# Optimization experiments

Measured on AMD Instinct MI355X. Metric: run time of the kernel, lower is better.

## Reference

```python
import jax, jax.numpy as jnp
import numpy as np

B, N, C = 8, 8192, 256
H, D, S = 8, 32, 32          # heads, dim_head, slice_num
HID = 4 * C                  # mlp hidden


def layernorm(x, w, b, eps=1e-5):
    mu = jnp.mean(x, axis=-1, keepdims=True)
    var = jnp.mean(jnp.square(x - mu), axis=-1, keepdims=True)
    return (x - mu) * jax.lax.rsqrt(var + eps) * w + b


def setup_inputs() -> dict:
    key = jax.random.key(0)
    ks = jax.random.split(key, 16)
    s = lambda fan: 1.0 / np.sqrt(fan)
    return {
        "fx": jax.random.normal(ks[0], (B, N, C), jnp.float32),
        "ln1_w": jnp.ones((C,), jnp.float32),
        "ln1_b": jnp.zeros((C,), jnp.float32),
        "Wx": jax.random.uniform(ks[1], (C, C), jnp.float32, -s(C), s(C)),   # in_project_x weight [inner,dim]
        "bx": jax.random.uniform(ks[2], (C,), jnp.float32, -s(C), s(C)),
        "Wq": jax.random.uniform(ks[3], (S, D), jnp.float32, -s(D), s(D)),
        "Wk": jax.random.uniform(ks[4], (S, D), jnp.float32, -s(D), s(D)),
        "Wv": jax.random.uniform(ks[5], (D, D), jnp.float32, -s(D), s(D)),
        "Wo": jax.random.uniform(ks[6], (C, C), jnp.float32, -s(C), s(C)),   # to_out weight [dim,inner]
        "bo": jax.random.uniform(ks[7], (C,), jnp.float32, -s(C), s(C)),
        "ln2_w": jnp.ones((C,), jnp.float32),
        "ln2_b": jnp.zeros((C,), jnp.float32),
        "W1": jax.random.uniform(ks[8], (HID, C), jnp.float32, -s(C), s(C)),
        "b1": jax.random.uniform(ks[9], (HID,), jnp.float32, -s(C), s(C)),
        "W2": jax.random.uniform(ks[10], (C, HID), jnp.float32, -s(HID), s(HID)),
        "b2": jax.random.uniform(ks[11], (C,), jnp.float32, -s(HID), s(HID)),
    }


def linear_no_attn(x, Wx, bx, Wq, Wk, Wv, Wo, bo):
    # x: [B,N,C]
    x_mid = x @ Wx.T + bx                                   # [B,N,C]
    x_mid = x_mid.reshape(x.shape[0], x.shape[1], H, D).transpose(0, 2, 1, 3)  # [B,H,N,D]
    q = jax.nn.softmax(x_mid @ Wq.T, axis=-1)               # [B,H,N,S], softmax over slices
    k = jax.nn.softmax(x_mid @ Wk.T, axis=-2)               # [B,H,N,S], softmax over tokens
    v = x_mid @ Wv.T                                        # [B,H,N,D]
    kv = jnp.einsum('bhns,bhnd->bhsd', k, v)                # [B,H,S,D]
    qkv = jnp.einsum('bhns,bhsd->bhnd', q, kv)              # [B,H,N,D]
    qkv = qkv.transpose(0, 2, 1, 3).reshape(x.shape[0], x.shape[1], H * D)
    return qkv @ Wo.T + bo


def reference(fx, ln1_w, ln1_b, Wx, bx, Wq, Wk, Wv, Wo, bo, ln2_w, ln2_b, W1, b1, W2, b2):
    h = linear_no_attn(layernorm(fx, ln1_w, ln1_b), Wx, bx, Wq, Wk, Wv, Wo, bo) + fx
    y = layernorm(h, ln2_w, ln2_b)
    y = jax.nn.gelu(y @ W1.T + b1, approximate=False)       # MLP: pre + exact GELU, n_layers=0
    y = y @ W2.T + b2
    return y + h
```

## Files before the change

kernel.cpp:

```cpp
#include <hip/hip_runtime.h>
#include <math.h>


typedef __attribute__((ext_vector_type(8))) short bf8;
typedef __attribute__((ext_vector_type(4))) float f32x4;
typedef __attribute__((ext_vector_type(4))) unsigned short u16x4;
typedef __attribute__((ext_vector_type(8))) unsigned short u16x8;

__device__ __forceinline__ float b2f(unsigned short x) {
  union { unsigned u; float f; } t; t.u = ((unsigned)x) << 16; return t.f;
}
__device__ __forceinline__ unsigned short f2b(float f) {
  union { float f; unsigned u; } t; t.f = f;
  unsigned r = t.u + 0x7fffu + ((t.u >> 16) & 1u);
  return (unsigned short)(r >> 16);
}
__device__ __forceinline__ float gelu_exact(float x) {
  return 0.5f * x * (1.0f + erff(x * 0.7071067811865475f));
}
__device__ __forceinline__ float erf_fast(float x) {
  float ax = fabsf(x);
  float t = __builtin_amdgcn_rcpf(fmaf(0.3275911f, ax, 1.0f));
  float p = t * fmaf(t, fmaf(t, fmaf(t, fmaf(t, 1.061405429f, -1.453152027f),
                                     1.421413741f), -0.284496736f), 0.254829592f);
  float r = 1.0f - p * __expf(-ax * ax);
  return copysignf(r, x);
}
__device__ __forceinline__ float gelu_fast(float x) {
  return 0.5f * x * (1.0f + erf_fast(x * 0.7071067811865475f));
}

typedef __attribute__((address_space(1))) const void gas_void;
typedef __attribute__((address_space(3))) void las_void;
__device__ __forceinline__ void gl_lds16(const void* g, void* l) {
  __builtin_amdgcn_global_load_lds((gas_void*)g, (las_void*)l, 16, 0, 0);
}

__global__ void sniff_kernel(const unsigned* __restrict__ fx, int* __restrict__ flag,
                             unsigned* __restrict__ gate) {
  if (threadIdx.x == 0) {
    int cnt = 0;
    for (int i = 0; i < 64; i++) {
      unsigned e = (fx[i] >> 7) & 0xFFu;
      cnt += (e >= 117u && e <= 130u) ? 1 : 0;
    }
    *flag = (cnt >= 32) ? 1 : 0;
    *gate = 0u;
  }
}

struct CvtDesc { const void* src[15]; int off[15]; int n[15]; };

__global__ __launch_bounds__(256) void cvt_tab(CvtDesc d, unsigned short* __restrict__ wtab,
                                               const int* __restrict__ flagp) {
  const int seg = blockIdx.y;
  const int i = blockIdx.x * 256 + threadIdx.x;
  if (i >= d.n[seg]) return;
  unsigned short o;
  if (*flagp) o = ((const unsigned short*)d.src[seg])[i];
  else        o = f2b(((const float*)d.src[seg])[i]);
  wtab[d.off[seg] + i] = o;
}

__global__ __launch_bounds__(256) void build_big(
    const unsigned short* __restrict__ wq, const unsigned short* __restrict__ wk,
    unsigned short* __restrict__ Wqbig, unsigned short* __restrict__ Wkbig)
{
  const int idx = blockIdx.x * 256 + threadIdx.x;
  const int row = idx >> 8, col = idx & 255;
  const bool same = (row >> 5) == (col >> 5);
  const int wi = (row & 31) * 32 + (col & 31);
  Wqbig[idx] = same ? wq[wi] : (unsigned short)0;
  Wkbig[idx] = same ? wk[wi] : (unsigned short)0;
}

__global__ __launch_bounds__(256) void zero_u16(unsigned short* __restrict__ p, int n) {
  int i8 = (blockIdx.x * 256 + threadIdx.x) * 8;
  if (i8 < n) { u16x8 z = {}; *(u16x8*)&p[i8] = z; }
}

__global__ __launch_bounds__(256) void ln_stats(
    const void* __restrict__ X, const int* __restrict__ flagp, int amode,
    float* __restrict__ MU, float* __restrict__ RS)
{
  const int lane = threadIdx.x & 63;
  const int wave = threadIdx.x >> 6;
  const size_t row = (size_t)blockIdx.x * 4 + wave;
  const size_t base = row * 256 + lane * 4;
  const bool abf = amode ? ((*flagp) != 0) : true;
  float x0, x1, x2, x3;
  if (abf) {
    u16x4 uv = *(const u16x4*)&((const unsigned short*)X)[base];
    x0 = b2f(uv[0]); x1 = b2f(uv[1]); x2 = b2f(uv[2]); x3 = b2f(uv[3]);
  } else {
    f32x4 t = *(const f32x4*)&((const float*)X)[base];
    x0 = t[0]; x1 = t[1]; x2 = t[2]; x3 = t[3];
  }
  float s = x0 + x1 + x2 + x3;
  float q = x0*x0 + x1*x1 + x2*x2 + x3*x3;
  #pragma unroll
  for (int m = 1; m < 64; m <<= 1) { s += __shfl_xor(s, m, 64); q += __shfl_xor(q, m, 64); }
  float mean = s * (1.0f / 256.0f);
  float var  = q * (1.0f / 256.0f) - mean * mean;
  if (lane == 0) { MU[row] = mean; RS[row] = rsqrtf(var + 1e-5f); }
}

__global__ __launch_bounds__(256) void gemm_bt(
    const unsigned short* __restrict__ A,
    const unsigned short* __restrict__ W,
    const unsigned short* __restrict__ bias,
    const void* __restrict__ Res, const int* __restrict__ flagp,
    unsigned short* __restrict__ Y,
    int N, int K, int act, int mz, long wz)
{
  __shared__ __align__(16) unsigned short smem[3 * 8192];
  const int tid = threadIdx.x, lane = tid & 63, wave = tid >> 6;
  const size_t zrow = (size_t)blockIdx.z * mz;
  const int bm = blockIdx.x * 128, bn = blockIdx.y * 128;
  const int wm = (wave >> 1) * 64, wn = (wave & 1) * 64;
  const int quad = lane >> 4, l16 = lane & 15;
  const unsigned short* Wz = W + (size_t)blockIdx.z * wz;

  f32x4 acc[4][4] = {};
  const int r0 = tid >> 2;
  const int co = (tid & 3) * 8;
  const unsigned short* pa0 = &A[(zrow + bm + r0) * K + co];
  const unsigned short* pa1 = &A[(zrow + bm + r0 + 64) * K + co];
  const unsigned short* pb0 = &Wz[(size_t)(bn + r0) * K + co];
  const unsigned short* pb1 = &Wz[(size_t)(bn + r0 + 64) * K + co];
  const int nt = K >> 5;

  auto stage = [&](int t, int sl) {
    const int k0 = t << 5;
    unsigned short* b_ = &smem[sl * 8192 + tid * 8];
    gl_lds16(pa0 + k0, b_);
    gl_lds16(pa1 + k0, b_ + 2048);
    gl_lds16(pb0 + k0, b_ + 4096);
    gl_lds16(pb1 + k0, b_ + 6144);
  };

  stage(0, 0);
  if (nt > 1) stage(1, 1);
  int scur = 0, snew = 2;
  for (int t = 0; t < nt; ++t) {
    if (t + 2 < nt) {
      stage(t + 2, snew);
      asm volatile("s_waitcnt vmcnt(8)" ::: "memory");
    } else if (t + 1 < nt) {
      asm volatile("s_waitcnt vmcnt(4)" ::: "memory");
    } else {
      asm volatile("s_waitcnt vmcnt(0)" ::: "memory");
    }
    __builtin_amdgcn_s_barrier();
    __builtin_amdgcn_sched_barrier(0);

    const unsigned short* sa = &smem[scur * 8192];
    const unsigned short* sb = sa + 4096;
    bf8 af[4], bfr[4];
    #pragma unroll
    for (int i = 0; i < 4; i++) af[i]  = *(const bf8*)&sa[(wm + i * 16 + l16) * 32 + quad * 8];
    #pragma unroll
    for (int j = 0; j < 4; j++) bfr[j] = *(const bf8*)&sb[(wn + j * 16 + l16) * 32 + quad * 8];
    #pragma unroll
    for (int i = 0; i < 4; i++)
      #pragma unroll
      for (int j = 0; j < 4; j++)
        acc[i][j] = __builtin_amdgcn_mfma_f32_16x16x32_bf16(af[i], bfr[j], acc[i][j], 0, 0, 0);

    __builtin_amdgcn_sched_barrier(0);
    __builtin_amdgcn_s_barrier();
    scur = scur + 1 < 3 ? scur + 1 : 0;
    snew = snew + 1 < 3 ? snew + 1 : 0;
  }

  const bool rbf = Res ? ((*flagp) != 0) : true;
  float bv[4];
  #pragma unroll
  for (int j = 0; j < 4; j++) bv[j] = b2f(bias[bn + wn + j * 16 + l16]);
  #pragma unroll
  for (int i = 0; i < 4; i++)
    #pragma unroll
    for (int j = 0; j < 4; j++)
      #pragma unroll
      for (int r = 0; r < 4; r++) {
        float v = acc[i][j][r] + bv[j];
        if (act == 2) v = __expf(v);
        acc[i][j][r] = v;
      }
  if (act == 3) {
    #pragma unroll
    for (int i = 0; i < 4; i++)
      #pragma unroll
      for (int g = 0; g < 2; g++)
        #pragma unroll
        for (int r = 0; r < 4; r++) {
          float a0 = acc[i][2*g][r], a1 = acc[i][2*g+1][r];
          float m = fmaxf(a0, a1);
          #pragma unroll
          for (int msk = 1; msk < 16; msk <<= 1) m = fmaxf(m, __shfl_xor(m, msk, 64));
          float e0 = __expf(a0 - m), e1 = __expf(a1 - m);
          float s = e0 + e1;
          #pragma unroll
          for (int msk = 1; msk < 16; msk <<= 1) s += __shfl_xor(s, msk, 64);
          const float rz = 1.0f / s;
          acc[i][2*g][r] = e0 * rz; acc[i][2*g+1][r] = e1 * rz;
        }
  }

  float* cf = (float*)smem;
  const int whalf = wm >> 6;
  #pragma unroll
  for (int half = 0; half < 2; ++half) {
    __builtin_amdgcn_s_barrier();
    if (whalf == half) {
      #pragma unroll
      for (int i = 0; i < 4; i++)
        #pragma unroll
        for (int j = 0; j < 4; j++)
          #pragma unroll
          for (int r = 0; r < 4; r++)
            cf[(i * 16 + quad * 4 + r) * 132 + wn + j * 16 + l16] = acc[i][j][r];
    }
    __builtin_amdgcn_s_barrier();
    #pragma unroll
    for (int st = 0; st < 4; ++st) {
      const int e = st * 2048 + tid * 8;
      const int row = e >> 7;
      const int col = e & 127;
      const size_t gbase = (zrow + bm + half * 64 + row) * (size_t)N + bn + col;
      float v[8];
      #pragma unroll
      for (int u = 0; u < 8; u++) v[u] = cf[row * 132 + col + u];
      if (Res) {
        if (rbf) {
          u16x8 rv = *(const u16x8*)&((const unsigned short*)Res)[gbase];
          #pragma unroll
          for (int u = 0; u < 8; u++) v[u] += b2f(rv[u]);
        } else {
          f32x4 ra = *(const f32x4*)&((const float*)Res)[gbase];
          f32x4 rb = *(const f32x4*)&((const float*)Res)[gbase + 4];
          v[0] += ra[0]; v[1] += ra[1]; v[2] += ra[2]; v[3] += ra[3];
          v[4] += rb[0]; v[5] += rb[1]; v[6] += rb[2]; v[7] += rb[3];
        }
      }
      u16x8 o;
      #pragma unroll
      for (int u = 0; u < 8; u++) o[u] = f2b(v[u]);
      *(u16x8*)&Y[gbase] = o;
    }
  }
}

__global__ __launch_bounds__(256) void gemm_bt_ln(
    const void* __restrict__ A, const int* __restrict__ flagp, int amode,
    const float* __restrict__ MU, const float* __restrict__ RS,
    const unsigned short* __restrict__ lw, const unsigned short* __restrict__ lb,
    const unsigned short* __restrict__ W, const unsigned short* __restrict__ bias,
    unsigned short* __restrict__ Y, int N, int K, int act)
{
  __shared__ __align__(16) unsigned char smemc[32768];
  unsigned short* lA = (unsigned short*)smemc;
  unsigned short* lB = lA + 4096;
  const int tid = threadIdx.x, lane = tid & 63, wave = tid >> 6;
  const int bm = blockIdx.x * 128, bn = blockIdx.y * 128;
  const int wm = (wave >> 1) * 64, wn = (wave & 1) * 64;
  const int quad = lane >> 4, l16 = lane & 15;
  const bool abf = amode ? ((*flagp) != 0) : true;
  const unsigned short* Ab = (const unsigned short*)A;
  const float* Af = (const float*)A;

  f32x4 acc[4][4] = {};
  const int r0 = tid >> 2;
  const int co = (tid & 3) * 8;
  const unsigned short* pb0 = &W[(size_t)(bn + r0) * K + co];
  const unsigned short* pb1 = &W[(size_t)(bn + r0 + 64) * K + co];

  for (int k0 = 0; k0 < K; k0 += 32) {
    u16x8 wv8 = *(const u16x8*)&lw[k0 + co];
    u16x8 bv8 = *(const u16x8*)&lb[k0 + co];
    __syncthreads();
    gl_lds16(pb0 + k0, &lB[tid * 8]);
    gl_lds16(pb1 + k0, &lB[2048 + tid * 8]);
    #pragma unroll
    for (int half = 0; half < 2; half++) {
      const int ar = bm + r0 + half * 64;
      const float m_ = MU[ar], r_ = RS[ar];
      float xv[8];
      if (abf) {
        u16x8 t = *(const u16x8*)&Ab[(size_t)ar * K + k0 + co];
        #pragma unroll
        for (int e = 0; e < 8; e++) xv[e] = b2f(t[e]);
      } else {
        f32x4 t0 = *(const f32x4*)&Af[(size_t)ar * K + k0 + co];
        f32x4 t1 = *(const f32x4*)&Af[(size_t)ar * K + k0 + co + 4];
        xv[0]=t0[0]; xv[1]=t0[1]; xv[2]=t0[2]; xv[3]=t0[3];
        xv[4]=t1[0]; xv[5]=t1[1]; xv[6]=t1[2]; xv[7]=t1[3];
      }
      u16x8 o;
      #pragma unroll
      for (int e = 0; e < 8; e++)
        o[e] = f2b((xv[e] - m_) * r_ * b2f(wv8[e]) + b2f(bv8[e]));
      *(u16x8*)&lA[half * 2048 + tid * 8] = o;
    }
    __syncthreads();

    bf8 af[4], bfr[4];
    #pragma unroll
    for (int i = 0; i < 4; i++) af[i]  = *(const bf8*)&lA[(wm + i * 16 + l16) * 32 + quad * 8];
    #pragma unroll
    for (int j = 0; j < 4; j++) bfr[j] = *(const bf8*)&lB[(wn + j * 16 + l16) * 32 + quad * 8];
    #pragma unroll
    for (int i = 0; i < 4; i++)
      #pragma unroll
      for (int j = 0; j < 4; j++)
        acc[i][j] = __builtin_amdgcn_mfma_f32_16x16x32_bf16(af[i], bfr[j], acc[i][j], 0, 0, 0);
  }

  float bv[4];
  #pragma unroll
  for (int j = 0; j < 4; j++) bv[j] = b2f(bias[bn + wn + j * 16 + l16]);
  #pragma unroll
  for (int i = 0; i < 4; i++)
    #pragma unroll
    for (int j = 0; j < 4; j++)
      #pragma unroll
      for (int r = 0; r < 4; r++) {
        float v = acc[i][j][r] + bv[j];
        if (act) v = gelu_exact(v);
        acc[i][j][r] = v;
      }

  float* cf = (float*)smemc;
  const int whalf = wm >> 6;
  #pragma unroll
  for (int half = 0; half < 2; ++half) {
    __syncthreads();
    if (whalf == half) {
      #pragma unroll
      for (int i = 0; i < 4; i++)
        #pragma unroll
        for (int j = 0; j < 4; j++)
          #pragma unroll
          for (int r = 0; r < 4; r++)
            cf[(i * 16 + quad * 4 + r) * 128 + wn + j * 16 + l16] = acc[i][j][r];
    }
    __syncthreads();
    #pragma unroll
    for (int st = 0; st < 4; ++st) {
      const int e = st * 2048 + tid * 8;
      const int row = e >> 7;
      const size_t gbase = (size_t)(bm + half * 64 + row) * N + bn + (e & 127);
      u16x8 o;
      #pragma unroll
      for (int u = 0; u < 8; u++) o[u] = f2b(cf[e + u]);
      *(u16x8*)&Y[gbase] = o;
    }
  }
}

__global__ __launch_bounds__(512, 2) void fused_mlp(
    const unsigned short* __restrict__ Hlo,
    const unsigned short* __restrict__ Hhi,
    const float* __restrict__ MU, const float* __restrict__ RS,
    const unsigned short* __restrict__ lw, const unsigned short* __restrict__ lb,
    const unsigned short* __restrict__ W1, const unsigned short* __restrict__ bs1,
    const unsigned short* __restrict__ W2, const unsigned short* __restrict__ bs2,
    void* __restrict__ OUT, const int* __restrict__ flagp,
    unsigned* __restrict__ gate)
{
  __shared__ __align__(16) unsigned char smem[104448];
  const int tid = threadIdx.x, lane = tid & 63, wave = tid >> 6;
  const int quad = lane >> 4, l16 = lane & 15;
  const int bid = blockIdx.x;
  const bool low = (bid & 1) == 0;
  const long grow = (low ? 0L : 32768L) + (long)(bid >> 1) * 256;
  const unsigned short* hbase = low ? (Hlo + (size_t)grow * 256)
                                    : (Hhi + ((size_t)grow - 32768) * 256);

  auto stageW1 = [&](int c, int sl) {
    const unsigned short* src = W1 + (size_t)c * 8192;
    unsigned char* dst = smem + sl * 16384;
    #pragma unroll
    for (int s = 0; s < 2; s++) {
      const int unit = s * 512 + tid;
      const int row = unit >> 5, u = unit & 31;
      gl_lds16(src + row * 256 + ((u ^ (row & 7)) * 8), dst + unit * 16);
    }
  };
  auto stageW2 = [&](int c, int sl) {
    const unsigned short* src = W2 + c * 32;
    unsigned char* dst = smem + 49152 + sl * 16384;
    #pragma unroll
    for (int s = 0; s < 2; s++) {
      const int unit = s * 512 + tid;
      const int row = unit >> 2, u = unit & 3;
      gl_lds16(src + (size_t)row * 1024 + ((u ^ ((row >> 1) & 3)) * 8), dst + unit * 16);
    }
  };

  unsigned short* b1l = (unsigned short*)(smem + 102400);
  if (tid < 128) *(u16x8*)&b1l[tid * 8] = *(const u16x8*)&bs1[tid * 8];

  bf8 areg[2][8];
  #pragma unroll
  for (int rg = 0; rg < 2; rg++) {
    const int myrow = wave * 32 + rg * 16 + l16;
    const float m_ = MU[grow + myrow], r_ = RS[grow + myrow];
    const unsigned short* hr = hbase + (size_t)myrow * 256 + quad * 8;
    #pragma unroll
    for (int ks = 0; ks < 8; ks++) {
      u16x8 hv = *(const u16x8*)&hr[ks * 32];
      u16x8 wv = *(const u16x8*)&lw[ks * 32 + quad * 8];
      u16x8 bv = *(const u16x8*)&lb[ks * 32 + quad * 8];
      u16x8 o;
      #pragma unroll
      for (int e = 0; e < 8; e++)
        o[e] = f2b((b2f(hv[e]) - m_) * r_ * b2f(wv[e]) + b2f(bv[e]));
      *(u16x8*)&areg[rg][ks] = o;
    }
  }
  asm volatile("s_waitcnt vmcnt(0) lgkmcnt(0)" ::: "memory");

  stageW1(0, 0); stageW2(0, 0);
  stageW1(1, 1); stageW2(1, 1);
  asm volatile("s_waitcnt vmcnt(4)" ::: "memory");
  __builtin_amdgcn_s_barrier();
  __builtin_amdgcn_sched_barrier(0);

  f32x4 p00 = {}, p01 = {}, p10 = {}, p11 = {};
  {
    const unsigned short* w1b = (const unsigned short*)smem;
    #pragma unroll
    for (int ks = 0; ks < 8; ks++) {
      const int slot = (ks * 4 + quad) ^ (l16 & 7);
      bf8 a0, a1;
      *(u16x8*)&a0 = *(const u16x8*)&w1b[l16 * 256 + slot * 8];
      *(u16x8*)&a1 = *(const u16x8*)&w1b[(16 + l16) * 256 + slot * 8];
      p00 = __builtin_amdgcn_mfma_f32_16x16x32_bf16(a0, areg[0][ks], p00, 0, 0, 0);
      p01 = __builtin_amdgcn_mfma_f32_16x16x32_bf16(a0, areg[1][ks], p01, 0, 0, 0);
      p10 = __builtin_amdgcn_mfma_f32_16x16x32_bf16(a1, areg[0][ks], p10, 0, 0, 0);
      p11 = __builtin_amdgcn_mfma_f32_16x16x32_bf16(a1, areg[1][ks], p11, 0, 0, 0);
    }
  }

  f32x4 acc[2][16] = {};
  unsigned short* tw = (unsigned short*)(smem + 81920 + wave * 2560);
  const int gsw = (l16 >> 1) & 3;

  for (int c = 0; c < 32; ++c) {
    if (c + 2 < 32) stageW1(c + 2, (c + 2) % 3);

    {
      u16x4 bv0 = *(const u16x4*)&b1l[c * 32 + quad * 4];
      u16x4 bv1 = *(const u16x4*)&b1l[c * 32 + 16 + quad * 4];
      u16x4 o00, o01, o10, o11;
      #pragma unroll
      for (int r = 0; r < 4; r++) {
        o00[r] = f2b(gelu_fast(p00[r] + b2f(bv0[r])));
        o01[r] = f2b(gelu_fast(p01[r] + b2f(bv0[r])));
        o10[r] = f2b(gelu_fast(p10[r] + b2f(bv1[r])));
        o11[r] = f2b(gelu_fast(p11[r] + b2f(bv1[r])));
      }
      *(u16x4*)&tw[l16 * 40 + quad * 4]             = o00;
      *(u16x4*)&tw[(16 + l16) * 40 + quad * 4]      = o01;
      *(u16x4*)&tw[l16 * 40 + 16 + quad * 4]        = o10;
      *(u16x4*)&tw[(16 + l16) * 40 + 16 + quad * 4] = o11;
    }
    asm volatile("s_waitcnt lgkmcnt(0)" ::: "memory");
    __builtin_amdgcn_sched_barrier(0);

    {
      bf8 ta0, ta1;
      *(u16x8*)&ta0 = *(const u16x8*)&tw[l16 * 40 + quad * 8];
      *(u16x8*)&ta1 = *(const u16x8*)&tw[(16 + l16) * 40 + quad * 8];
      const unsigned short* w2b = (const unsigned short*)(smem + 49152 + (c & 1) * 16384);
      #pragma unroll
      for (int j = 0; j < 16; j++) {
        bf8 bw;
        *(u16x8*)&bw = *(const u16x8*)&w2b[(j * 16 + l16) * 32 + ((quad ^ gsw) * 8)];
        acc[0][j] = __builtin_amdgcn_mfma_f32_16x16x32_bf16(ta0, bw, acc[0][j], 0, 0, 0);
        acc[1][j] = __builtin_amdgcn_mfma_f32_16x16x32_bf16(ta1, bw, acc[1][j], 0, 0, 0);
      }
    }

    if (c + 2 < 32) asm volatile("s_waitcnt vmcnt(2)" ::: "memory");
    else            asm volatile("s_waitcnt vmcnt(0)" ::: "memory");
    __builtin_amdgcn_s_barrier();
    __builtin_amdgcn_sched_barrier(0);

    if (c + 2 < 32) stageW2(c + 2, (c + 2) & 1);
    if (c + 1 < 32) {
      const unsigned short* w1b = (const unsigned short*)(smem + ((c + 1) % 3) * 16384);
      p00 = {}; p01 = {}; p10 = {}; p11 = {};
      #pragma unroll
      for (int ks = 0; ks < 8; ks++) {
        const int slot = (ks * 4 + quad) ^ (l16 & 7);
        bf8 a0, a1;
        *(u16x8*)&a0 = *(const u16x8*)&w1b[l16 * 256 + slot * 8];
        *(u16x8*)&a1 = *(const u16x8*)&w1b[(16 + l16) * 256 + slot * 8];
        p00 = __builtin_amdgcn_mfma_f32_16x16x32_bf16(a0, areg[0][ks], p00, 0, 0, 0);
        p01 = __builtin_amdgcn_mfma_f32_16x16x32_bf16(a0, areg[1][ks], p01, 0, 0, 0);
        p10 = __builtin_amdgcn_mfma_f32_16x16x32_bf16(a1, areg[0][ks], p10, 0, 0, 0);
        p11 = __builtin_amdgcn_mfma_f32_16x16x32_bf16(a1, areg[1][ks], p11, 0, 0, 0);
      }
    }
  }

  if (!low) {
    if (tid == 0) {
      while (__hip_atomic_load(gate, __ATOMIC_ACQUIRE, __HIP_MEMORY_SCOPE_AGENT) < 128u)
        __builtin_amdgcn_s_sleep(32);
    }
    __syncthreads();
  }

  const bool obf = (*flagp) != 0;
  float* cf = (float*)smem;
  #pragma unroll
  for (int q = 0; q < 4; ++q) {
    __syncthreads();
    if ((wave >> 1) == q) {
      const int wl = (wave & 1) * 32;
      #pragma unroll
      for (int rg = 0; rg < 2; rg++)
        #pragma unroll
        for (int j = 0; j < 16; j++)
          #pragma unroll
          for (int r = 0; r < 4; r++)
            cf[(wl + rg * 16 + quad * 4 + r) * 260 + j * 16 + l16] = acc[rg][j][r];
    }
    __syncthreads();
    const unsigned short* hrow = hbase + (size_t)(q * 64) * 256;
    #pragma unroll
    for (int s = 0; s < 4; s++) {
      const int e = s * 4096 + tid * 8;
      const int row = e >> 8, col = e & 255;
      u16x8 rv = *(const u16x8*)&hrow[e];
      u16x8 b2v = *(const u16x8*)&bs2[col];
      float v[8];
      #pragma unroll
      for (int u = 0; u < 8; u++) v[u] = cf[row * 260 + col + u] + b2f(rv[u]) + b2f(b2v[u]);
      const size_t ob = (size_t)(grow + q * 64 + row) * 256 + col;
      if (obf) {
        u16x8 o;
        #pragma unroll
        for (int u = 0; u < 8; u++) o[u] = f2b(v[u]);
        *(u16x8*)&((unsigned short*)OUT)[ob] = o;
      } else {
        f32x4 oa, obv;
        oa[0]=v[0]; oa[1]=v[1]; oa[2]=v[2]; oa[3]=v[3];
        obv[0]=v[4]; obv[1]=v[5]; obv[2]=v[6]; obv[3]=v[7];
        *(f32x4*)&((float*)OUT)[ob] = oa;
        *(f32x4*)&((float*)OUT)[ob + 4] = obv;
      }
    }
  }

  if (low) {
    __syncthreads();
    if (tid == 0)
      __hip_atomic_fetch_add(gate, 1u, __ATOMIC_RELEASE, __HIP_MEMORY_SCOPE_AGENT);
  }
}

__global__ __launch_bounds__(256) void accumG(
    const unsigned short* __restrict__ X,
    const unsigned short* __restrict__ E,
    float* __restrict__ Gp)
{
  __shared__ float Xl[64 * 256];
  __shared__ __align__(16) unsigned short El[64 * 256];
  const int tid = threadIdx.x;
  const int k = blockIdx.x;
  const int h = tid >> 5, s = tid & 31;

  float acc[32];
  #pragma unroll
  for (int d = 0; d < 32; d++) acc[d] = 0.f;
  float zacc = 0.f;

  for (int sub = 0; sub < 4; sub++) {
    const size_t r0s = (size_t)k * 256 + sub * 64;
    __syncthreads();
    #pragma unroll
    for (int i = 0; i < 8; i++) {
      const int flat = i * 2048 + tid * 8;
      u16x8 xv = *(const u16x8*)&X[r0s * 256 + flat];
      #pragma unroll
      for (int e = 0; e < 8; e++) Xl[flat + e] = b2f(xv[e]);
      *(u16x8*)&El[flat] = *(const u16x8*)&E[r0s * 256 + flat];
    }
    __syncthreads();

    for (int t = 0; t < 64; t++) {
      const float e = b2f(El[t * 256 + h * 32 + s]);
      zacc += e;
      const int xb = t * 256 + h * 32;
      #pragma unroll
      for (int dq = 0; dq < 8; dq++) {
        f32x4 xv = *(const f32x4*)&Xl[xb + dq * 4];
        acc[dq*4+0] += e * xv[0];
        acc[dq*4+1] += e * xv[1];
        acc[dq*4+2] += e * xv[2];
        acc[dq*4+3] += e * xv[3];
      }
    }
  }

  float* gp = &Gp[(size_t)k * 8448 + (size_t)tid * 32];
  #pragma unroll
  for (int dq = 0; dq < 8; dq++) {
    f32x4 o; o[0]=acc[dq*4]; o[1]=acc[dq*4+1]; o[2]=acc[dq*4+2]; o[3]=acc[dq*4+3];
    *(f32x4*)&gp[dq * 4] = o;
  }
  Gp[(size_t)k * 8448 + 8192 + tid] = zacc;
}

__global__ __launch_bounds__(256) void reduceG(const float* __restrict__ Gp,
                                               float* __restrict__ Gfin) {
  const int o = blockIdx.x * 256 + threadIdx.x;
  if (o >= 67584) return;
  const int b = o / 8448;
  const int j = o - b * 8448;
  float s = 0.f;
  #pragma unroll 8
  for (int i = 0; i < 32; i++) s += Gp[(size_t)(b * 32 + i) * 8448 + j];
  Gfin[o] = s;
}

__global__ __launch_bounds__(256) void kv_build(
    const float* __restrict__ Gfin, const unsigned short* __restrict__ Wv,
    unsigned short* __restrict__ KVB)
{
  __shared__ float Gl[8192];
  __shared__ float zl[256];
  __shared__ float wvt[1024];
  const int tid = threadIdx.x;
  const int b = blockIdx.x;
  for (int i = tid; i < 8192; i += 256) Gl[i] = Gfin[(size_t)b * 8448 + i];
  zl[tid] = Gfin[(size_t)b * 8448 + 8192 + tid];
  for (int i = tid; i < 1024; i += 256) {
    const int dd = i >> 5, d = i & 31;
    wvt[i] = b2f(Wv[d * 32 + dd]);
  }
  __syncthreads();

  const int h = tid >> 5, d = tid & 31;
  unsigned short row[32];
  for (int s = 0; s < 32; s++) {
    float a = 0.f;
    #pragma unroll
    for (int dd = 0; dd < 32; dd++) a += Gl[h * 1024 + s * 32 + dd] * wvt[dd * 32 + d];
    row[s] = f2b(a / zl[h * 32 + s]);
  }
  unsigned short* out = &KVB[(size_t)b * 65536 + (size_t)(h * 32 + d) * 256 + h * 32];
  #pragma unroll
  for (int e = 0; e < 4; e++) *(u16x8*)&out[e * 8] = *(u16x8*)&row[e * 8];
}

__global__ __launch_bounds__(256) void copy_h0(const unsigned short* __restrict__ src,
                                               unsigned short* __restrict__ dst) {
  size_t i = ((size_t)blockIdx.x * 256 + threadIdx.x) * 8;
  *(u16x8*)&dst[i] = *(const u16x8*)&src[i];
}

extern "C" void kernel_launch(void* const* d_in, const int* in_sizes, int n_in,
                              void* d_out, int out_size, void* d_ws, size_t ws_size,
                              hipStream_t stream)
{
  const void* fx   = d_in[0];
  const void* ln1w = d_in[1];
  const void* ln1b = d_in[2];
  const void* Wx   = d_in[3];
  const void* bx   = d_in[4];
  const void* Wq   = d_in[5];
  const void* Wk   = d_in[6];
  const void* Wv   = d_in[7];
  const void* Wo   = d_in[8];
  const void* bo   = d_in[9];
  const void* ln2w = d_in[10];
  const void* ln2b = d_in[11];
  const void* W1   = d_in[12];
  const void* b1   = d_in[13];
  const void* W2   = d_in[14];
  const void* b2   = d_in[15];

  unsigned short* ws    = (unsigned short*)d_ws;
  unsigned short* hid   = ws;
  float* Gp             = (float*)ws;
  unsigned short* wtab  = ws + 8388608;
  unsigned short* h0res = wtab + 661248;
  float* Gfin           = (float*)h0res;
  unsigned short* Wqbig = h0res + 2097152;
  unsigned short* Wkbig = Wqbig + 65536;
  unsigned short* KVB   = Wkbig + 65536;
  unsigned short* zbias = KVB + 524288;
  float* fpw = (float*)(zbias + 256);
  float* mu1 = fpw;
  float* rs1 = fpw + 65536;
  float* mu2 = fpw + 131072;
  float* rs2 = fpw + 196608;
  int* flagp = (int*)(fpw + 262144);
  unsigned* gatep = (unsigned*)(flagp + 1);

  const int OFF_LN1W=0, OFF_LN1B=256, OFF_WX=512, OFF_BX=66048,
            OFF_WQ=66304, OFF_WK=67328, OFF_WV=68352,
            OFF_WO=69376, OFF_BO=134912, OFF_LN2W=135168, OFF_LN2B=135424,
            OFF_W1=135680, OFF_B1=397824, OFF_W2=398848, OFF_B2=660992;

  unsigned short* xm  = (unsigned short*)d_out;
  unsigned short* xup = xm + 16777216;

  sniff_kernel<<<1, 64, 0, stream>>>((const unsigned*)fx, flagp, gatep);
  CvtDesc cd;
  const void* srcs[15] = {ln1w, ln1b, Wx, bx, Wq, Wk, Wv, Wo, bo, ln2w, ln2b, W1, b1, W2, b2};
  const int offs[15]   = {OFF_LN1W, OFF_LN1B, OFF_WX, OFF_BX, OFF_WQ, OFF_WK, OFF_WV,
                          OFF_WO, OFF_BO, OFF_LN2W, OFF_LN2B, OFF_W1, OFF_B1, OFF_W2, OFF_B2};
  const int ns[15]     = {256, 256, 65536, 256, 1024, 1024, 1024, 65536, 256, 256, 256,
                          262144, 1024, 262144, 256};
  for (int i = 0; i < 15; i++) { cd.src[i] = srcs[i]; cd.off[i] = offs[i]; cd.n[i] = ns[i]; }
  cvt_tab<<<dim3(1024, 15), 256, 0, stream>>>(cd, wtab, flagp);
  build_big<<<256, 256, 0, stream>>>(wtab + OFF_WQ, wtab + OFF_WK, Wqbig, Wkbig);
  zero_u16<<<257, 256, 0, stream>>>(KVB, 524544);

  ln_stats<<<16384, 256, 0, stream>>>(fx, flagp, 1, mu1, rs1);
  gemm_bt_ln<<<dim3(512, 2), 256, 0, stream>>>(fx, flagp, 1, mu1, rs1,
      wtab + OFF_LN1W, wtab + OFF_LN1B, wtab + OFF_WX, wtab + OFF_BX,
      xm, 256, 256, 0);

  gemm_bt<<<dim3(512, 2), 256, 0, stream>>>(xm, Wkbig, zbias, nullptr, flagp,
                                            xup, 256, 256, 2, 0, 0);

  accumG<<<256, 256, 0, stream>>>(xm, xup, Gp);
  reduceG<<<264, 256, 0, stream>>>(Gp, Gfin);
  kv_build<<<8, 256, 0, stream>>>(Gfin, wtab + OFF_WV, KVB);

  gemm_bt<<<dim3(512, 2), 256, 0, stream>>>(xm, Wqbig, zbias, nullptr, flagp,
                                            xup, 256, 256, 3, 0, 0);

  gemm_bt<<<dim3(64, 2, 8), 256, 0, stream>>>(xup, KVB, zbias, nullptr, flagp,
                                              xm, 256, 256, 0, 8192, 65536);

  gemm_bt<<<dim3(512, 2), 256, 0, stream>>>(xm, wtab + OFF_WO, wtab + OFF_BO, fx, flagp,
                                            xup, 256, 256, 0, 0, 0);

  ln_stats<<<16384, 256, 0, stream>>>(xup, flagp, 0, mu2, rs2);
  copy_h0<<<4096, 256, 0, stream>>>(xup + (size_t)32768 * 256, hid);

  fused_mlp<<<256, 512, 0, stream>>>(xup, hid, mu2, rs2,
      wtab + OFF_LN2W, wtab + OFF_LN2B, wtab + OFF_W1, wtab + OFF_B1,
      wtab + OFF_W2, wtab + OFF_B2, d_out, flagp, gatep);
}
```

Measured before the change: 485.3 us.

## Fuse q-softmax, kv product and output projection into one per-tile kernel

Replaces the block-diagonal padded Wq/Wk GEMMs and the separate KV and Wo GEMMs with a single kernel. Per row tile it computes q logits per head, applies the slice softmax, multiplies by a compact per-batch KV, and accumulates the Wo projection with bias and residual, so the intermediates never go to global memory. The k projection and its exp are also folded into accumG, computed in registers from Wk, which removes the exp GEMM and its buffer. Padded weight building and zeroing kernels go away. The cost is a more register- and LDS-heavy fused kernel with per-head serial steps and redundant k-dot work in accumG.

Result: slower. 559.1 us (+15.2%).

```diff
diff --git a/kernel.cpp b/kernel.cpp
--- a/kernel.cpp
+++ b/kernel.cpp
@@ -60,23 +60,6 @@
   if (*flagp) o = ((const unsigned short*)d.src[seg])[i];
   else        o = f2b(((const float*)d.src[seg])[i]);
   wtab[d.off[seg] + i] = o;
-}
-
-__global__ __launch_bounds__(256) void build_big(
-    const unsigned short* __restrict__ wq, const unsigned short* __restrict__ wk,
-    unsigned short* __restrict__ Wqbig, unsigned short* __restrict__ Wkbig)
-{
-  const int idx = blockIdx.x * 256 + threadIdx.x;
-  const int row = idx >> 8, col = idx & 255;
-  const bool same = (row >> 5) == (col >> 5);
-  const int wi = (row & 31) * 32 + (col & 31);
-  Wqbig[idx] = same ? wq[wi] : (unsigned short)0;
-  Wkbig[idx] = same ? wk[wi] : (unsigned short)0;
-}
-
-__global__ __launch_bounds__(256) void zero_u16(unsigned short* __restrict__ p, int n) {
-  int i8 = (blockIdx.x * 256 + threadIdx.x) * 8;
-  if (i8 < n) { u16x8 z = {}; *(u16x8*)&p[i8] = z; }
 }
 
 __global__ __launch_bounds__(256) void ln_stats(
@@ -103,152 +86,6 @@
   float mean = s * (1.0f / 256.0f);
   float var  = q * (1.0f / 256.0f) - mean * mean;
   if (lane == 0) { MU[row] = mean; RS[row] = rsqrtf(var + 1e-5f); }
-}
-
-__global__ __launch_bounds__(256) void gemm_bt(
-    const unsigned short* __restrict__ A,
-    const unsigned short* __restrict__ W,
-    const unsigned short* __restrict__ bias,
-    const void* __restrict__ Res, const int* __restrict__ flagp,
-    unsigned short* __restrict__ Y,
-    int N, int K, int act, int mz, long wz)
-{
-  __shared__ __align__(16) unsigned short smem[3 * 8192];
-  const int tid = threadIdx.x, lane = tid & 63, wave = tid >> 6;
-  const size_t zrow = (size_t)blockIdx.z * mz;
-  const int bm = blockIdx.x * 128, bn = blockIdx.y * 128;
-  const int wm = (wave >> 1) * 64, wn = (wave & 1) * 64;
-  const int quad = lane >> 4, l16 = lane & 15;
-  const unsigned short* Wz = W + (size_t)blockIdx.z * wz;
-
-  f32x4 acc[4][4] = {};
-  const int r0 = tid >> 2;
-  const int co = (tid & 3) * 8;
-  const unsigned short* pa0 = &A[(zrow + bm + r0) * K + co];
-  const unsigned short* pa1 = &A[(zrow + bm + r0 + 64) * K + co];
-  const unsigned short* pb0 = &Wz[(size_t)(bn + r0) * K + co];
-  const unsigned short* pb1 = &Wz[(size_t)(bn + r0 + 64) * K + co];
-  const int nt = K >> 5;
-
-  auto stage = [&](int t, int sl) {
-    const int k0 = t << 5;
-    unsigned short* b_ = &smem[sl * 8192 + tid * 8];
-    gl_lds16(pa0 + k0, b_);
-    gl_lds16(pa1 + k0, b_ + 2048);
-    gl_lds16(pb0 + k0, b_ + 4096);
-    gl_lds16(pb1 + k0, b_ + 6144);
-  };
-
-  stage(0, 0);
-  if (nt > 1) stage(1, 1);
-  int scur = 0, snew = 2;
-  for (int t = 0; t < nt; ++t) {
-    if (t + 2 < nt) {
-      stage(t + 2, snew);
-      asm volatile("s_waitcnt vmcnt(8)" ::: "memory");
-    } else if (t + 1 < nt) {
-      asm volatile("s_waitcnt vmcnt(4)" ::: "memory");
-    } else {
-      asm volatile("s_waitcnt vmcnt(0)" ::: "memory");
-    }
-    __builtin_amdgcn_s_barrier();
-    __builtin_amdgcn_sched_barrier(0);
-
-    const unsigned short* sa = &smem[scur * 8192];
-    const unsigned short* sb = sa + 4096;
-    bf8 af[4], bfr[4];
-    #pragma unroll
-    for (int i = 0; i < 4; i++) af[i]  = *(const bf8*)&sa[(wm + i * 16 + l16) * 32 + quad * 8];
-    #pragma unroll
-    for (int j = 0; j < 4; j++) bfr[j] = *(const bf8*)&sb[(wn + j * 16 + l16) * 32 + quad * 8];
-    #pragma unroll
-    for (int i = 0; i < 4; i++)
-      #pragma unroll
-      for (int j = 0; j < 4; j++)
-        acc[i][j] = __builtin_amdgcn_mfma_f32_16x16x32_bf16(af[i], bfr[j], acc[i][j], 0, 0, 0);
-
-    __builtin_amdgcn_sched_barrier(0);
-    __builtin_amdgcn_s_barrier();
-    scur = scur + 1 < 3 ? scur + 1 : 0;
-    snew = snew + 1 < 3 ? snew + 1 : 0;
-  }
-
-  const bool rbf = Res ? ((*flagp) != 0) : true;
-  float bv[4];
-  #pragma unroll
-  for (int j = 0; j < 4; j++) bv[j] = b2f(bias[bn + wn + j * 16 + l16]);
-  #pragma unroll
-  for (int i = 0; i < 4; i++)
-    #pragma unroll
-    for (int j = 0; j < 4; j++)
-      #pragma unroll
-      for (int r = 0; r < 4; r++) {
-        float v = acc[i][j][r] + bv[j];
-        if (act == 2) v = __expf(v);
-        acc[i][j][r] = v;
-      }
-  if (act == 3) {
-    #pragma unroll
-    for (int i = 0; i < 4; i++)
-      #pragma unroll
-      for (int g = 0; g < 2; g++)
-        #pragma unroll
-        for (int r = 0; r < 4; r++) {
-          float a0 = acc[i][2*g][r], a1 = acc[i][2*g+1][r];
-          float m = fmaxf(a0, a1);
-          #pragma unroll
-          for (int msk = 1; msk < 16; msk <<= 1) m = fmaxf(m, __shfl_xor(m, msk, 64));
-          float e0 = __expf(a0 - m), e1 = __expf(a1 - m);
-          float s = e0 + e1;
-          #pragma unroll
-          for (int msk = 1; msk < 16; msk <<= 1) s += __shfl_xor(s, msk, 64);
-          const float rz = 1.0f / s;
-          acc[i][2*g][r] = e0 * rz; acc[i][2*g+1][r] = e1 * rz;
-        }
-  }
-
-  float* cf = (float*)smem;
-  const int whalf = wm >> 6;
-  #pragma unroll
-  for (int half = 0; half < 2; ++half) {
-    __builtin_amdgcn_s_barrier();
-    if (whalf == half) {
-      #pragma unroll
-      for (int i = 0; i < 4; i++)
-        #pragma unroll
-        for (int j = 0; j < 4; j++)
-          #pragma unroll
-          for (int r = 0; r < 4; r++)
-            cf[(i * 16 + quad * 4 + r) * 132 + wn + j * 16 + l16] = acc[i][j][r];
-    }
-    __builtin_amdgcn_s_barrier();
-    #pragma unroll
-    for (int st = 0; st < 4; ++st) {
-      const int e = st * 2048 + tid * 8;
-      const int row = e >> 7;
-      const int col = e & 127;
-      const size_t gbase = (zrow + bm + half * 64 + row) * (size_t)N + bn + col;
-      float v[8];
-      #pragma unroll
-      for (int u = 0; u < 8; u++) v[u] = cf[row * 132 + col + u];
-      if (Res) {
-        if (rbf) {
-          u16x8 rv = *(const u16x8*)&((const unsigned short*)Res)[gbase];
-          #pragma unroll
-          for (int u = 0; u < 8; u++) v[u] += b2f(rv[u]);
-        } else {
-          f32x4 ra = *(const f32x4*)&((const float*)Res)[gbase];
-          f32x4 rb = *(const f32x4*)&((const float*)Res)[gbase + 4];
-          v[0] += ra[0]; v[1] += ra[1]; v[2] += ra[2]; v[3] += ra[3];
-          v[4] += rb[0]; v[5] += rb[1]; v[6] += rb[2]; v[7] += rb[3];
-        }
-      }
-      u16x8 o;
-      #pragma unroll
-      for (int u = 0; u < 8; u++) o[u] = f2b(v[u]);
-      *(u16x8*)&Y[gbase] = o;
-    }
-  }
 }
 
 __global__ __launch_bounds__(256) void gemm_bt_ln(
@@ -354,6 +191,189 @@
       #pragma unroll
       for (int u = 0; u < 8; u++) o[u] = f2b(cf[e + u]);
       *(u16x8*)&Y[gbase] = o;
+    }
+  }
+}
+
+__global__ __launch_bounds__(256, 2) void qkvwo(
+    const unsigned short* __restrict__ Xm,
+    const unsigned short* __restrict__ wq,
+    const unsigned short* __restrict__ kvTg,
+    const unsigned short* __restrict__ Wo,
+    const unsigned short* __restrict__ bo,
+    const void* __restrict__ Fx, const int* __restrict__ flagp,
+    unsigned short* __restrict__ Hout)
+{
+  __shared__ __align__(16) unsigned char smem[73728];
+  const int tid = threadIdx.x, lane = tid & 63, wave = tid >> 6;
+  const int quad = lane >> 4, l16 = lane & 15;
+  const int brow = blockIdx.x * 128;
+  const int b = brow >> 13;
+
+  if (tid < 128) {
+    const int row = tid >> 2, u = tid & 3;
+    gl_lds16(wq + row * 32 + ((u ^ ((row >> 1) & 3)) * 8), smem + tid * 16);
+  }
+  {
+    const unsigned short* src = kvTg + (size_t)b * 8192;
+    #pragma unroll
+    for (int s = 0; s < 4; s++) {
+      const int unit = s * 256 + tid;
+      const int row = unit >> 2, u = unit & 3;
+      gl_lds16(src + row * 32 + ((u ^ ((row >> 1) & 3)) * 8), smem + 4096 + unit * 16);
+    }
+  }
+  auto stageWo = [&](int hh, int slot) {
+    const unsigned short* src = Wo + hh * 32;
+    unsigned char* dst = smem + 20480 + slot * 16384;
+    #pragma unroll
+    for (int s = 0; s < 4; s++) {
+      const int unit = s * 256 + tid;
+      const int row = unit >> 2, u = unit & 3;
+      gl_lds16(src + row * 256 + ((u ^ ((row >> 1) & 3)) * 8), dst + unit * 16);
+    }
+  };
+  stageWo(0, 0);
+
+  bf8 areg[2][8];
+  #pragma unroll
+  for (int rg = 0; rg < 2; rg++) {
+    const int myrow = wave * 32 + rg * 16 + l16;
+    const unsigned short* hr = Xm + (size_t)(brow + myrow) * 256 + quad * 8;
+    #pragma unroll
+    for (int ks = 0; ks < 8; ks++)
+      *(u16x8*)&areg[rg][ks] = *(const u16x8*)&hr[ks * 32];
+  }
+
+  asm volatile("s_waitcnt vmcnt(0) lgkmcnt(0)" ::: "memory");
+  __builtin_amdgcn_s_barrier();
+  __builtin_amdgcn_sched_barrier(0);
+
+  f32x4 acc[2][16] = {};
+  unsigned short* tw1 = (unsigned short*)(smem + 53248 + wave * 5120);
+  unsigned short* tw2 = tw1 + 1280;
+  const unsigned short* wql = (const unsigned short*)smem;
+  const unsigned short* kvl = (const unsigned short*)(smem + 4096);
+
+  #pragma unroll
+  for (int h = 0; h < 8; ++h) {
+    if (h < 7) stageWo(h + 1, (h + 1) & 1);
+
+    f32x4 p[2][2] = {{{}, {}}, {{}, {}}};
+    #pragma unroll
+    for (int jl = 0; jl < 2; jl++) {
+      const int row = jl * 16 + l16;
+      bf8 wqf;
+      *(u16x8*)&wqf = *(const u16x8*)&wql[row * 32 + ((quad ^ ((row >> 1) & 3)) * 8)];
+      p[0][jl] = __builtin_amdgcn_mfma_f32_16x16x32_bf16(areg[0][h], wqf, p[0][jl], 0, 0, 0);
+      p[1][jl] = __builtin_amdgcn_mfma_f32_16x16x32_bf16(areg[1][h], wqf, p[1][jl], 0, 0, 0);
+    }
+
+    #pragma unroll
+    for (int rg = 0; rg < 2; rg++)
+      #pragma unroll
+      for (int r = 0; r < 4; r++) {
+        float a0 = p[rg][0][r], a1 = p[rg][1][r];
+        float m = fmaxf(a0, a1);
+        #pragma unroll
+        for (int msk = 1; msk < 16; msk <<= 1) m = fmaxf(m, __shfl_xor(m, msk, 64));
+        float e0 = __expf(a0 - m), e1 = __expf(a1 - m);
+        float s = e0 + e1;
+        #pragma unroll
+        for (int msk = 1; msk < 16; msk <<= 1) s += __shfl_xor(s, msk, 64);
+        const float rz = 1.0f / s;
+        const int row = rg * 16 + quad * 4 + r;
+        tw1[row * 40 + l16]      = f2b(e0 * rz);
+        tw1[row * 40 + 16 + l16] = f2b(e1 * rz);
+      }
+    asm volatile("s_waitcnt lgkmcnt(0)" ::: "memory");
+    __builtin_amdgcn_sched_barrier(0);
+
+    bf8 ta0, ta1;
+    *(u16x8*)&ta0 = *(const u16x8*)&tw1[l16 * 40 + quad * 8];
+    *(u16x8*)&ta1 = *(const u16x8*)&tw1[(16 + l16) * 40 + quad * 8];
+    asm volatile("s_waitcnt lgkmcnt(0)" ::: "memory");
+    __builtin_amdgcn_sched_barrier(0);
+    f32x4 p2[2][2] = {{{}, {}}, {{}, {}}};
+    #pragma unroll
+    for (int jd = 0; jd < 2; jd++) {
+      const int row = h * 32 + jd * 16 + l16;
+      bf8 kvf;
+      *(u16x8*)&kvf = *(const u16x8*)&kvl[row * 32 + ((quad ^ ((row >> 1) & 3)) * 8)];
+      p2[0][jd] = __builtin_amdgcn_mfma_f32_16x16x32_bf16(ta0, kvf, p2[0][jd], 0, 0, 0);
+      p2[1][jd] = __builtin_amdgcn_mfma_f32_16x16x32_bf16(ta1, kvf, p2[1][jd], 0, 0, 0);
+    }
+
+    #pragma unroll
+    for (int rg = 0; rg < 2; rg++)
+      #pragma unroll
+      for (int jd = 0; jd < 2; jd++)
+        #pragma unroll
+        for (int r = 0; r < 4; r++)
+          tw2[(rg * 16 + quad * 4 + r) * 40 + jd * 16 + l16] = f2b(p2[rg][jd][r]);
+    asm volatile("s_waitcnt lgkmcnt(0)" ::: "memory");
+    __builtin_amdgcn_sched_barrier(0);
+
+    bf8 a20, a21;
+    *(u16x8*)&a20 = *(const u16x8*)&tw2[l16 * 40 + quad * 8];
+    *(u16x8*)&a21 = *(const u16x8*)&tw2[(16 + l16) * 40 + quad * 8];
+    asm volatile("s_waitcnt lgkmcnt(0)" ::: "memory");
+    __builtin_amdgcn_sched_barrier(0);
+
+    const unsigned short* wol = (const unsigned short*)(smem + 20480 + (h & 1) * 16384);
+    #pragma unroll
+    for (int j = 0; j < 16; j++) {
+      const int row = j * 16 + l16;
+      bf8 bw;
+      *(u16x8*)&bw = *(const u16x8*)&wol[row * 32 + ((quad ^ ((row >> 1) & 3)) * 8)];
+      acc[0][j] = __builtin_amdgcn_mfma_f32_16x16x32_bf16(a20, bw, acc[0][j], 0, 0, 0);
+      acc[1][j] = __builtin_amdgcn_mfma_f32_16x16x32_bf16(a21, bw, acc[1][j], 0, 0, 0);
+    }
+
+    asm volatile("s_waitcnt vmcnt(0)" ::: "memory");
+    __builtin_amdgcn_s_barrier();
+    __builtin_amdgcn_sched_barrier(0);
+  }
+
+  const bool rbf = (*flagp) != 0;
+  float* cf = (float*)smem;
+  #pragma unroll
+  for (int hh = 0; hh < 2; ++hh) {
+    __syncthreads();
+    if ((wave >> 1) == hh) {
+      const int wl = (wave & 1) * 32;
+      #pragma unroll
+      for (int rg = 0; rg < 2; rg++)
+        #pragma unroll
+        for (int j = 0; j < 16; j++)
+          #pragma unroll
+          for (int r = 0; r < 4; r++)
+            cf[(wl + rg * 16 + quad * 4 + r) * 260 + j * 16 + l16] = acc[rg][j][r];
+    }
+    __syncthreads();
+    #pragma unroll
+    for (int s = 0; s < 8; s++) {
+      const int e = s * 2048 + tid * 8;
+      const int row = e >> 8, col = e & 255;
+      const size_t gbase = (size_t)(brow + hh * 64 + row) * 256 + col;
+      u16x8 bv = *(const u16x8*)&bo[col];
+      float v[8];
+      #pragma unroll
+      for (int u = 0; u < 8; u++) v[u] = cf[row * 260 + col + u] + b2f(bv[u]);
+      if (rbf) {
+        u16x8 rv = *(const u16x8*)&((const unsigned short*)Fx)[gbase];
+        #pragma unroll
+        for (int u = 0; u < 8; u++) v[u] += b2f(rv[u]);
+      } else {
+        f32x4 ra = *(const f32x4*)&((const float*)Fx)[gbase];
+        f32x4 rb = *(const f32x4*)&((const float*)Fx)[gbase + 4];
+        v[0] += ra[0]; v[1] += ra[1]; v[2] += ra[2]; v[3] += ra[3];
+        v[4] += rb[0]; v[5] += rb[1]; v[6] += rb[2]; v[7] += rb[3];
+      }
+      u16x8 o;
+      #pragma unroll
+      for (int u = 0; u < 8; u++) o[u] = f2b(v[u]);
+      *(u16x8*)&Hout[gbase] = o;
     }
   }
 }
@@ -565,15 +585,22 @@
 
 __global__ __launch_bounds__(256) void accumG(
     const unsigned short* __restrict__ X,
-    const unsigned short* __restrict__ E,
+    const unsigned short* __restrict__ wk,
     float* __restrict__ Gp)
 {
   __shared__ float Xl[64 * 256];
-  __shared__ __align__(16) unsigned short El[64 * 256];
   const int tid = threadIdx.x;
   const int k = blockIdx.x;
   const int h = tid >> 5, s = tid & 31;
 
+  float wkr[32];
+  #pragma unroll
+  for (int d4 = 0; d4 < 4; d4++) {
+    u16x8 wv = *(const u16x8*)&wk[s * 32 + d4 * 8];
+    #pragma unroll
+    for (int e = 0; e < 8; e++) wkr[d4 * 8 + e] = b2f(wv[e]);
+  }
+
   float acc[32];
   #pragma unroll
   for (int d = 0; d < 32; d++) acc[d] = 0.f;
@@ -588,21 +615,30 @@
       u16x8 xv = *(const u16x8*)&X[r0s * 256 + flat];
       #pragma unroll
       for (int e = 0; e < 8; e++) Xl[flat + e] = b2f(xv[e]);
-      *(u16x8*)&El[flat] = *(const u16x8*)&E[r0s * 256 + flat];
     }
     __syncthreads();
 
     for (int t = 0; t < 64; t++) {
-      const float e = b2f(El[t * 256 + h * 32 + s]);
+      const int xb = t * 256 + h * 32;
+      f32x4 xv[8];
+      #pragma unroll
+      for (int dq = 0; dq < 8; dq++) xv[dq] = *(const f32x4*)&Xl[xb + dq * 4];
+      float dot = 0.f;
+      #pragma unroll
+      for (int dq = 0; dq < 8; dq++) {
+        dot = fmaf(wkr[dq*4+0], xv[dq][0], dot);
+        dot = fmaf(wkr[dq*4+1], xv[dq][1], dot);
+        dot = fmaf(wkr[dq*4+2], xv[dq][2], dot);
+        dot = fmaf(wkr[dq*4+3], xv[dq][3], dot);
+      }
+      const float e = __expf(dot);
       zacc += e;
-      const int xb = t * 256 + h * 32;
       #pragma unroll
       for (int dq = 0; dq < 8; dq++) {
-        f32x4 xv = *(const f32x4*)&Xl[xb + dq * 4];
-        acc[dq*4+0] += e * xv[0];
-        acc[dq*4+1] += e * xv[1];
-        acc[dq*4+2] += e * xv[2];
-        acc[dq*4+3] += e * xv[3];
+        acc[dq*4+0] = fmaf(e, xv[dq][0], acc[dq*4+0]);
+        acc[dq*4+1] = fmaf(e, xv[dq][1], acc[dq*4+1]);
+        acc[dq*4+2] = fmaf(e, xv[dq][2], acc[dq*4+2]);
+        acc[dq*4+3] = fmaf(e, xv[dq][3], acc[dq*4+3]);
       }
     }
   }
@@ -630,7 +666,7 @@
 
 __global__ __launch_bounds__(256) void kv_build(
     const float* __restrict__ Gfin, const unsigned short* __restrict__ Wv,
-    unsigned short* __restrict__ KVB)
+    unsigned short* __restrict__ KVT)
 {
   __shared__ float Gl[8192];
   __shared__ float zl[256];
@@ -653,7 +689,7 @@
     for (int dd = 0; dd < 32; dd++) a += Gl[h * 1024 + s * 32 + dd] * wvt[dd * 32 + d];
     row[s] = f2b(a / zl[h * 32 + s]);
   }
-  unsigned short* out = &KVB[(size_t)b * 65536 + (size_t)(h * 32 + d) * 256 + h * 32];
+  unsigned short* out = &KVT[(size_t)b * 8192 + (size_t)(h * 32 + d) * 32];
   #pragma unroll
   for (int e = 0; e < 4; e++) *(u16x8*)&out[e * 8] = *(u16x8*)&row[e * 8];
 }
@@ -691,11 +727,8 @@
   unsigned short* wtab  = ws + 8388608;
   unsigned short* h0res = wtab + 661248;
   float* Gfin           = (float*)h0res;
-  unsigned short* Wqbig = h0res + 2097152;
-  unsigned short* Wkbig = Wqbig + 65536;
-  unsigned short* KVB   = Wkbig + 65536;
-  unsigned short* zbias = KVB + 524288;
-  float* fpw = (float*)(zbias + 256);
+  unsigned short* kvT   = h0res + 2097152 + 131072;
+  float* fpw = (float*)(kvT + 524288);
   float* mu1 = fpw;
   float* rs1 = fpw + 65536;
   float* mu2 = fpw + 131072;
@@ -720,29 +753,18 @@
                           262144, 1024, 262144, 256};
   for (int i = 0; i < 15; i++) { cd.src[i] = srcs[i]; cd.off[i] = offs[i]; cd.n[i] = ns[i]; }
   cvt_tab<<<dim3(1024, 15), 256, 0, stream>>>(cd, wtab, flagp);
-  build_big<<<256, 256, 0, stream>>>(wtab + OFF_WQ, wtab + OFF_WK, Wqbig, Wkbig);
-  zero_u16<<<257, 256, 0, stream>>>(KVB, 524544);
 
   ln_stats<<<16384, 256, 0, stream>>>(fx, flagp, 1, mu1, rs1);
   gemm_bt_ln<<<dim3(512, 2), 256, 0, stream>>>(fx, flagp, 1, mu1, rs1,
       wtab + OFF_LN1W, wtab + OFF_LN1B, wtab + OFF_WX, wtab + OFF_BX,
       xm, 256, 256, 0);
 
-  gemm_bt<<<dim3(512, 2), 256, 0, stream>>>(xm, Wkbig, zbias, nullptr, flagp,
-                                            xup, 256, 256, 2, 0, 0);
-
-  accumG<<<256, 256, 0, stream>>>(xm, xup, Gp);
+  accumG<<<256, 256, 0, stream>>>(xm, wtab + OFF_WK, Gp);
   reduceG<<<264, 256, 0, stream>>>(Gp, Gfin);
-  kv_build<<<8, 256, 0, stream>>>(Gfin, wtab + OFF_WV, KVB);
-
-  gemm_bt<<<dim3(512, 2), 256, 0, stream>>>(xm, Wqbig, zbias, nullptr, flagp,
-                                            xup, 256, 256, 3, 0, 0);
-
-  gemm_bt<<<dim3(64, 2, 8), 256, 0, stream>>>(xup, KVB, zbias, nullptr, flagp,
-                                              xm, 256, 256, 0, 8192, 65536);
-
-  gemm_bt<<<dim3(512, 2), 256, 0, stream>>>(xm, wtab + OFF_WO, wtab + OFF_BO, fx, flagp,
-                                            xup, 256, 256, 0, 0, 0);
+  kv_build<<<8, 256, 0, stream>>>(Gfin, wtab + OFF_WV, kvT);
+
+  qkvwo<<<512, 256, 0, stream>>>(xm, wtab + OFF_WQ, kvT, wtab + OFF_WO,
+                                 wtab + OFF_BO, fx, flagp, xup);
 
   ln_stats<<<16384, 256, 0, stream>>>(xup, flagp, 0, mu2, rs2);
   copy_h0<<<4096, 256, 0, stream>>>(xup + (size_t)32768 * 256, hid);
```
